# Kernel optimization log

Hardware: AMD Instinct MI355X
Metric: run time of the kernel (lower is better)

## Reference

```python
import jax, jax.numpy as jnp
import numpy as np

N = 40000
E = 640000
D_RNA = 1000
D_PROT = 300
H = 64      # hidden_channels
OUT = 32    # out_channels
HEADS = 4


def setup_inputs() -> dict:
    key = jax.random.key(0)
    ks = jax.random.split(key, 24)
    s = 0.05
    w = lambda k, shape: jax.random.normal(k, shape, jnp.float32) * s
    inp = {
        'x': jax.random.normal(ks[0], (N, D_RNA + D_PROT), jnp.float32),
        'edge_index': jax.random.randint(ks[1], (2, E), 0, N, jnp.int32),
        'input_dim_rna': D_RNA,
        # embeddings
        'W_rna': w(ks[2], (D_RNA, H)), 'b_rna': jnp.zeros((H,), jnp.float32),
        'W_prot': w(ks[3], (D_PROT, H)), 'b_prot': jnp.zeros((H,), jnp.float32),
        # GATConv1: in 2H=128 -> heads*H=256
        'W1s': w(ks[4], (2 * H, HEADS * H)), 'W1d': w(ks[5], (2 * H, HEADS * H)),
        'att1_s': w(ks[6], (HEADS, H)), 'att1_d': w(ks[7], (HEADS, H)),
        'bias1': jnp.zeros((HEADS * H,), jnp.float32),
        # lin1: 2H -> heads*H
        'Wl1': w(ks[8], (2 * H, HEADS * H)), 'bl1': jnp.zeros((HEADS * H,), jnp.float32),
        # GATConv2: in heads*H=256 -> heads*OUT=128
        'W2s': w(ks[9], (HEADS * H, HEADS * OUT)), 'W2d': w(ks[10], (HEADS * H, HEADS * OUT)),
        'att2_s': w(ks[11], (HEADS, OUT)), 'att2_d': w(ks[12], (HEADS, OUT)),
        'bias2': jnp.zeros((HEADS * OUT,), jnp.float32),
        # lin2: heads*H -> heads*OUT
        'Wl2': w(ks[13], (HEADS * H, HEADS * OUT)), 'bl2': jnp.zeros((HEADS * OUT,), jnp.float32),
    }
    return inp


def _gat(x_in, edge_index, Ws, Wd, att_s, att_d, bias, heads, ch):
    # PyG GATConv, bipartite weights, add_self_loops=False, concat=True, eval (no dropout)
    n = x_in.shape[0]
    src, dst = edge_index[0], edge_index[1]
    xs = (x_in @ Ws).reshape(n, heads, ch)   # source projection
    xd = (x_in @ Wd).reshape(n, heads, ch)   # destination projection
    a_s = jnp.einsum('nhc,hc->nh', xs, att_s)  # [N,H]
    a_d = jnp.einsum('nhc,hc->nh', xd, att_d)  # [N,H]
    e = jax.nn.leaky_relu(a_s[src] + a_d[dst], 0.2)          # [E,H]
    m = jax.lax.stop_gradient(jax.ops.segment_max(e, dst, num_segments=n))
    p = jnp.exp(e - m[dst])
    denom = jax.ops.segment_sum(p, dst, num_segments=n)       # [N,H]
    alpha = p / denom[dst]                                    # segment softmax over incoming edges
    msg = xs[src] * alpha[:, :, None]                         # [E,H,C]
    agg = jax.ops.segment_sum(msg, dst, num_segments=n)       # [N,H,C]
    return agg.reshape(n, heads * ch) + bias


def reference(x, edge_index, input_dim_rna, W_rna, b_rna, W_prot, b_prot,
              W1s, W1d, att1_s, att1_d, bias1, Wl1, bl1,
              W2s, W2d, att2_s, att2_d, bias2, Wl2, bl2):
    x_rna = x[:, :input_dim_rna] @ W_rna + b_rna
    x_prot = x[:, input_dim_rna:] @ W_prot + b_prot
    h = jnp.concatenate([x_rna, x_prot], axis=1)              # [N, 2H]
    h = _gat(h, edge_index, W1s, W1d, att1_s, att1_d, bias1, HEADS, H) + h @ Wl1 + bl1
    h = jax.nn.relu(h)
    out = _gat(h, edge_index, W2s, W2d, att2_s, att2_d, bias2, HEADS, OUT) + h @ Wl2 + bl2
    return out
```

## Files before the change

kernel.cpp:

```cpp
#include <hip/hip_runtime.h>
#include <hip/hip_bf16.h>
#include <stdint.h>


#define HEADS 4
#define CH1   64
#define CH2   32
#define HC1   256
#define HC2   128

static constexpr int D_RNA  = 1000;
static constexpr int D_PROT = 300;
static constexpr int D_IN   = 1300;
static constexpr int HDIM   = 128;

typedef __bf16 bf16x8 __attribute__((ext_vector_type(8)));
typedef float  f32x4  __attribute__((ext_vector_type(4)));
typedef unsigned short ushort;

__device__ __forceinline__ float lrelu(float x) { return x >= 0.f ? x : 0.2f * x; }
__device__ __forceinline__ float bf2f(unsigned int u16) {
  return __uint_as_float(u16 << 16);
}
__device__ __forceinline__ ushort f2bf(float f) {
  union { float f; unsigned int u; } x; x.f = f;
  unsigned int r = x.u + 0x7fffu + ((x.u >> 16) & 1u);
  return (ushort)(r >> 16);
}

__global__ void zero_i32(int* p, int n) {
  int i = blockIdx.x * 256 + threadIdx.x;
  if (i < n) p[i] = 0;
}

__global__ void hist_kernel(const int* __restrict__ dstv, int* __restrict__ deg, int E) {
  int i = blockIdx.x * 256 + threadIdx.x;
  if (i < E) atomicAdd(&deg[dstv[i]], 1);
}

__global__ void scan_kernel(const int* __restrict__ deg, int* __restrict__ off,
                            int* __restrict__ cur, int n) {
  __shared__ int s[1024];
  int tid = threadIdx.x;
  const int CHK = (n + 1023) / 1024;
  int base = tid * CHK;
  int sum = 0;
  for (int j = 0; j < CHK; ++j) {
    int i = base + j;
    if (i < n) sum += deg[i];
  }
  s[tid] = sum;
  __syncthreads();
  for (int o = 1; o < 1024; o <<= 1) {
    int t = (tid >= o) ? s[tid - o] : 0;
    __syncthreads();
    s[tid] += t;
    __syncthreads();
  }
  int run = s[tid] - sum;
  for (int j = 0; j < CHK; ++j) {
    int i = base + j;
    if (i < n) {
      off[i] = run; cur[i] = run;
      run += deg[i];
    }
  }
  if (tid == 1023) off[n] = s[1023];
}

__global__ void scatter_kernel(const int* __restrict__ srcv, const int* __restrict__ dstv,
                               int* __restrict__ cur, int* __restrict__ srcs, int E) {
  int i = blockIdx.x * 256 + threadIdx.x;
  if (i < E) {
    int d = dstv[i];
    int pos = atomicAdd(&cur[d], 1);
    srcs[pos] = srcv[i];
  }
}

__global__ void fold_att_kernel(const float* __restrict__ W1s, const float* __restrict__ W1d,
                                const float* __restrict__ at1s, const float* __restrict__ at1d,
                                const float* __restrict__ W2s, const float* __restrict__ W2d,
                                const float* __restrict__ at2s, const float* __restrict__ at2d,
                                ushort* __restrict__ BTA1, ushort* __restrict__ BTA2) {
  int tid = blockIdx.x * blockDim.x + threadIdx.x;
  int stride = gridDim.x * blockDim.x;
  for (int o = tid; o < HDIM * HEADS; o += stride) {
    int k = o >> 2, h = o & 3;
    float ss = 0.f, sd = 0.f;
    for (int c = 0; c < CH1; ++c) {
      ss += W1s[k * HC1 + h * CH1 + c] * at1s[h * CH1 + c];
      sd += W1d[k * HC1 + h * CH1 + c] * at1d[h * CH1 + c];
    }
    ushort sh = f2bf(ss), dh = f2bf(sd);
    BTA1[(0 + h) * HDIM + k] = sh;
    BTA1[(4 + h) * HDIM + k] = f2bf(ss - bf2f(sh));
    BTA1[(8 + h) * HDIM + k] = dh;
    BTA1[(12 + h) * HDIM + k] = f2bf(sd - bf2f(dh));
  }
  for (int o = tid; o < HC1 * HEADS; o += stride) {
    int k = o >> 2, h = o & 3;
    float ss = 0.f, sd = 0.f;
    for (int c = 0; c < CH2; ++c) {
      ss += W2s[k * HC2 + h * CH2 + c] * at2s[h * CH2 + c];
      sd += W2d[k * HC2 + h * CH2 + c] * at2d[h * CH2 + c];
    }
    ushort sh = f2bf(ss), dh = f2bf(sd);
    BTA2[(0 + h) * HC1 + k] = sh;
    BTA2[(4 + h) * HC1 + k] = f2bf(ss - bf2f(sh));
    BTA2[(8 + h) * HC1 + k] = dh;
    BTA2[(12 + h) * HC1 + k] = f2bf(sd - bf2f(dh));
  }
  for (int i = tid; i < 48 * HDIM; i += stride) BTA1[16 * HDIM + i] = 0;
  for (int i = tid; i < 48 * HC1; i += stride) BTA2[16 * HC1 + i] = 0;
}

__global__ void convert_weights(const float* __restrict__ W_rna, const float* __restrict__ W_prot,
                                const float* __restrict__ W1s, const float* __restrict__ Wl1,
                                const float* __restrict__ W2s, const float* __restrict__ Wl2,
                                const float* __restrict__ b1, const float* __restrict__ bl1,
                                const float* __restrict__ b2, const float* __restrict__ bl2,
                                ushort* BTr, ushort* BTp, ushort* BT1, ushort* BT2,
                                float* biasL1, float* biasL2) {
  int tid = blockIdx.x * blockDim.x + threadIdx.x;
  int stride = gridDim.x * blockDim.x;
  for (int i = tid; i < 64 * 1024; i += stride) {
    int n = i >> 10, k = i & 1023;
    BTr[i] = (k < D_RNA) ? f2bf(W_rna[k * 64 + n]) : 0;
  }
  for (int i = tid; i < 64 * 320; i += stride) {
    int n = i / 320, k = i - n * 320;
    BTp[i] = (k < D_PROT) ? f2bf(W_prot[k * 64 + n]) : 0;
  }
  for (int i = tid; i < 512 * 128; i += stride) {
    int n = i >> 7, k = i & 127;
    BT1[i] = f2bf(n < 256 ? W1s[k * 256 + n] : Wl1[k * 256 + n - 256]);
  }
  for (int i = tid; i < 256 * 256; i += stride) {
    int n = i >> 8, k = i & 255;
    BT2[i] = f2bf(n < 128 ? W2s[k * 128 + n] : Wl2[k * 128 + n - 128]);
  }
  for (int i = tid; i < 512; i += stride) biasL1[i] = (i < 256) ? b1[i] : bl1[i - 256];
  for (int i = tid; i < 256; i += stride) biasL2[i] = (i < 128) ? b2[i] : bl2[i - 128];
}

#define LDK 72

__device__ __forceinline__ f32x4 mfma_bf16(bf16x8 a, bf16x8 b, f32x4 c) {
  return __builtin_amdgcn_mfma_f32_16x16x32_bf16(a, b, c, 0, 0, 0);
}

__launch_bounds__(256)
__global__ void embed_gemm(const float* __restrict__ x,
                           const ushort* __restrict__ BTr, const ushort* __restrict__ BTp,
                           const float* __restrict__ b_rna, const float* __restrict__ b_prot,
                           ushort* __restrict__ h0) {
  const bool prot = (blockIdx.x == 1);
  const int Kpad = prot ? 320 : 1024;
  const int acol = prot ? D_RNA : 0;
  const ushort* BT = prot ? BTp : BTr;
  const float* bias = prot ? b_prot : b_rna;
  const int r0 = blockIdx.y * 64;

  __shared__ ushort As[64 * LDK];
  __shared__ ushort Bs[64 * LDK];
  int tid = threadIdx.x;
  int wave = tid >> 6, lane = tid & 63;
  int quad = lane >> 4, lr = lane & 15;
  f32x4 acc[4];
#pragma unroll
  for (int c = 0; c < 4; ++c) acc[c] = (f32x4){0.f, 0.f, 0.f, 0.f};

  int srow = tid >> 2, skq = (tid & 3) * 16;
  const float* aprow = x + (size_t)(r0 + srow) * D_IN;
  const ushort* bprow = BT + (size_t)srow * Kpad;

  float4 fa[4];
  uint4 fb0, fb1;

  auto loadA = [&](int k0) {
#pragma unroll
    for (int q = 0; q < 4; ++q) {
      int kg = acol + k0 + skq + q * 4;
      fa[q] = (kg + 4 <= D_IN) ? *(const float4*)(aprow + kg)
                               : make_float4(0.f, 0.f, 0.f, 0.f);
    }
  };
  auto loadB = [&](int k0) {
    const ushort* bp = bprow + k0 + skq;
    fb0 = *(const uint4*)bp;
    fb1 = *(const uint4*)(bp + 8);
  };

  loadA(0);
  loadB(0);

  for (int k0 = 0; k0 < Kpad; k0 += 64) {
    {
      ushort tmp[16];
#pragma unroll
      for (int q = 0; q < 4; ++q) {
        tmp[q * 4 + 0] = f2bf(fa[q].x); tmp[q * 4 + 1] = f2bf(fa[q].y);
        tmp[q * 4 + 2] = f2bf(fa[q].z); tmp[q * 4 + 3] = f2bf(fa[q].w);
      }
      *(uint4*)&As[srow * LDK + skq] = *(const uint4*)&tmp[0];
      *(uint4*)&As[srow * LDK + skq + 8] = *(const uint4*)&tmp[8];
      *(uint4*)&Bs[srow * LDK + skq] = fb0;
      *(uint4*)&Bs[srow * LDK + skq + 8] = fb1;
    }
    __syncthreads();
    if (k0 + 64 < Kpad) {
      loadA(k0 + 64);
      loadB(k0 + 64);
    }
    int arow = wave * 16 + lr;
    bf16x8 a0 = *(const bf16x8*)&As[arow * LDK + quad * 8];
    bf16x8 a1 = *(const bf16x8*)&As[arow * LDK + 32 + quad * 8];
#pragma unroll
    for (int c = 0; c < 4; ++c) {
      bf16x8 b0 = *(const bf16x8*)&Bs[(c * 16 + lr) * LDK + quad * 8];
      bf16x8 b1 = *(const bf16x8*)&Bs[(c * 16 + lr) * LDK + 32 + quad * 8];
      acc[c] = mfma_bf16(a0, b0, acc[c]);
      acc[c] = mfma_bf16(a1, b1, acc[c]);
    }
    __syncthreads();
  }
  int colb = prot ? 64 : 0;
#pragma unroll
  for (int c = 0; c < 4; ++c) {
#pragma unroll
    for (int j = 0; j < 4; ++j) {
      int row = r0 + wave * 16 + quad * 4 + j;
      int col = c * 16 + lr;
      h0[(size_t)row * HDIM + colb + col] = f2bf(acc[c][j] + bias[col]);
    }
  }
}

__launch_bounds__(256)
__global__ void layer_gemm(const ushort* __restrict__ A, int K,
                           const ushort* __restrict__ BT, const float* __restrict__ bias,
                           ushort* __restrict__ out0, ushort* __restrict__ out1, int halfw,
                           const ushort* __restrict__ BTA,
                           float* __restrict__ a_s, float* __restrict__ a_d) {
  const bool att = (blockIdx.x == gridDim.x - 1);
  const int cb = att ? 0 : blockIdx.x * 128;
  const int r0 = blockIdx.y * 64;
  __shared__ ushort As[64 * LDK];
  __shared__ ushort Bs[2][64 * LDK];
  int tid = threadIdx.x;
  int wave = tid >> 6, lane = tid & 63;
  int quad = lane >> 4, lr = lane & 15;
  f32x4 acc[8];
#pragma unroll
  for (int c = 0; c < 8; ++c) acc[c] = (f32x4){0.f, 0.f, 0.f, 0.f};

  int srow = tid >> 2, skq = (tid & 3) * 16;
  const ushort* aprow = A + (size_t)(r0 + srow) * K;
  const ushort* bprow0 = att ? (BTA + (size_t)srow * K)
                             : (BT + (size_t)(cb + srow) * K);
  const ushort* bprow1 = BT + (size_t)(cb + 64 + srow) * K;

  uint4 fa0, fa1, fb00, fb01, fb10, fb11;
  auto loadAB = [&](int k0) {
    const ushort* ap = aprow + k0 + skq;
    fa0 = *(const uint4*)ap;
    fa1 = *(const uint4*)(ap + 8);
    const ushort* bp0 = bprow0 + k0 + skq;
    fb00 = *(const uint4*)bp0;
    fb01 = *(const uint4*)(bp0 + 8);
    if (!att) {
      const ushort* bp1 = bprow1 + k0 + skq;
      fb10 = *(const uint4*)bp1;
      fb11 = *(const uint4*)(bp1 + 8);
    }
  };

  loadAB(0);

  for (int k0 = 0; k0 < K; k0 += 64) {
    *(uint4*)&As[srow * LDK + skq] = fa0;
    *(uint4*)&As[srow * LDK + skq + 8] = fa1;
    *(uint4*)&Bs[0][srow * LDK + skq] = fb00;
    *(uint4*)&Bs[0][srow * LDK + skq + 8] = fb01;
    if (!att) {
      *(uint4*)&Bs[1][srow * LDK + skq] = fb10;
      *(uint4*)&Bs[1][srow * LDK + skq + 8] = fb11;
    }
    __syncthreads();
    if (k0 + 64 < K) loadAB(k0 + 64);
    int arow = wave * 16 + lr;
    bf16x8 a0 = *(const bf16x8*)&As[arow * LDK + quad * 8];
    bf16x8 a1 = *(const bf16x8*)&As[arow * LDK + 32 + quad * 8];
#pragma unroll
    for (int c = 0; c < 4; ++c) {
      bf16x8 b0 = *(const bf16x8*)&Bs[0][(c * 16 + lr) * LDK + quad * 8];
      bf16x8 b1 = *(const bf16x8*)&Bs[0][(c * 16 + lr) * LDK + 32 + quad * 8];
      acc[c] = mfma_bf16(a0, b0, acc[c]);
      acc[c] = mfma_bf16(a1, b1, acc[c]);
    }
    if (!att) {
#pragma unroll
      for (int c = 0; c < 4; ++c) {
        bf16x8 b0 = *(const bf16x8*)&Bs[1][(c * 16 + lr) * LDK + quad * 8];
        bf16x8 b1 = *(const bf16x8*)&Bs[1][(c * 16 + lr) * LDK + 32 + quad * 8];
        acc[4 + c] = mfma_bf16(a0, b0, acc[4 + c]);
        acc[4 + c] = mfma_bf16(a1, b1, acc[4 + c]);
      }
    }
    __syncthreads();
  }
  if (att) {
#pragma unroll
    for (int j = 0; j < 4; ++j) {
      int row = r0 + wave * 16 + quad * 4 + j;
      float v0 = acc[0][j];
      float sum = v0 + __shfl_xor(v0, 4);
      if (lr < 4)                    a_s[(size_t)row * 4 + lr] = sum;
      else if (lr >= 8 && lr < 12)   a_d[(size_t)row * 4 + (lr - 8)] = sum;
    }
    return;
  }
#pragma unroll
  for (int t = 0; t < 2; ++t) {
#pragma unroll
    for (int c = 0; c < 4; ++c) {
#pragma unroll
      for (int j = 0; j < 4; ++j) {
        int row = r0 + wave * 16 + quad * 4 + j;
        int cg = cb + t * 64 + c * 16 + lr;
        ushort v = f2bf(acc[t * 4 + c][j] + bias[cg]);
        if (cg < halfw) out0[(size_t)row * halfw + cg] = v;
        else            out1[(size_t)row * halfw + cg - halfw] = v;
      }
    }
  }
}

__device__ __forceinline__ void load_bf8(const ushort* p, float* o) {
  uint4 q = *(const uint4*)p;
  o[0] = bf2f(q.x & 0xffffu); o[1] = bf2f(q.x >> 16);
  o[2] = bf2f(q.y & 0xffffu); o[3] = bf2f(q.y >> 16);
  o[4] = bf2f(q.z & 0xffffu); o[5] = bf2f(q.z >> 16);
  o[6] = bf2f(q.w & 0xffffu); o[7] = bf2f(q.w >> 16);
}

template <int CH, bool RELU, bool OUT_BF16>
__launch_bounds__(256)
__global__ void gat_fused_kernel(const int* __restrict__ off, const int* __restrict__ srcs,
                                 const float* __restrict__ a_s, const float* __restrict__ a_d,
                                 const ushort* __restrict__ xs,
                                 const float* __restrict__ bias,
                                 const ushort* __restrict__ skip,
                                 void* __restrict__ outv, int N) {
  const int HC  = 4 * CH;
  const int LPH = CH / 8;
  const int LPN = 4 * LPH;
  const int NPW = 64 / LPN;
  int wave = threadIdx.x >> 6, lane = threadIdx.x & 63;
  int g  = lane / LPN;
  int hl = (lane % LPN) / LPH;
  int li = lane % LPH;
  int n = blockIdx.x * (4 * NPW) + wave * NPW + g;
  if (n >= N) return;
  int i = off[n], end = off[n + 1];
  float adn = a_d[(size_t)n * 4 + hl];
  const int cofs = hl * CH + li * 8;

  float m = -1e30f, s = 0.f;
  float acc[8];
#pragma unroll
  for (int v = 0; v < 8; ++v) acc[v] = 0.f;

  for (; i + 2 <= end; i += 2) {
    int sA = srcs[i], sB = srcs[i + 1];
    float eA = lrelu(a_s[(size_t)sA * 4 + hl] + adn);
    float eB = lrelu(a_s[(size_t)sB * 4 + hl] + adn);
    float xA[8], xB[8];
    load_bf8(xs + (size_t)sA * HC + cofs, xA);
    load_bf8(xs + (size_t)sB * HC + cofs, xB);
    float mn = fmaxf(m, fmaxf(eA, eB));
    if (mn > m) {
      float f = __expf(m - mn);
      s *= f;
#pragma unroll
      for (int v = 0; v < 8; ++v) acc[v] *= f;
      m = mn;
    }
    float pA = __expf(eA - m), pB = __expf(eB - m);
    s += pA + pB;
#pragma unroll
    for (int v = 0; v < 8; ++v) acc[v] += pA * xA[v] + pB * xB[v];
  }
  if (i < end) {
    int sA = srcs[i];
    float eA = lrelu(a_s[(size_t)sA * 4 + hl] + adn);
    float xA[8];
    load_bf8(xs + (size_t)sA * HC + cofs, xA);
    if (eA > m) {
      float f = __expf(m - eA);
      s *= f;
#pragma unroll
      for (int v = 0; v < 8; ++v) acc[v] *= f;
      m = eA;
    }
    float pA = __expf(eA - m);
    s += pA;
#pragma unroll
    for (int v = 0; v < 8; ++v) acc[v] += pA * xA[v];
  }

  float r = s > 0.f ? 1.f / s : 0.f;
  size_t obase = (size_t)n * HC + cofs;
  float sk[8];
  load_bf8(skip + obase, sk);
  float val[8];
#pragma unroll
  for (int v = 0; v < 8; ++v) {
    val[v] = acc[v] * r + bias[cofs + v] + sk[v];
    if (RELU) val[v] = fmaxf(val[v], 0.f);
  }
  if (OUT_BF16) {
    ushort o8[8];
#pragma unroll
    for (int v = 0; v < 8; ++v) o8[v] = f2bf(val[v]);
    *(uint4*)&((ushort*)outv)[obase] = *(const uint4*)o8;
  } else {
    float* op = (float*)outv + obase;
    *(float4*)op = make_float4(val[0], val[1], val[2], val[3]);
    *(float4*)(op + 4) = make_float4(val[4], val[5], val[6], val[7]);
  }
}

extern "C" void kernel_launch(void* const* d_in, const int* in_sizes, int n_in,
                              void* d_out, int out_size, void* d_ws, size_t ws_size,
                              hipStream_t stream) {
  const float* x      = (const float*)d_in[0];
  const int*   ei     = (const int*)d_in[1];
  const float* W_rna  = (const float*)d_in[3];
  const float* b_rna  = (const float*)d_in[4];
  const float* W_prot = (const float*)d_in[5];
  const float* b_prot = (const float*)d_in[6];
  const float* W1s    = (const float*)d_in[7];
  const float* W1d    = (const float*)d_in[8];
  const float* at1s   = (const float*)d_in[9];
  const float* at1d   = (const float*)d_in[10];
  const float* bias1  = (const float*)d_in[11];
  const float* Wl1    = (const float*)d_in[12];
  const float* bl1    = (const float*)d_in[13];
  const float* W2s    = (const float*)d_in[14];
  const float* W2d    = (const float*)d_in[15];
  const float* at2s   = (const float*)d_in[16];
  const float* at2d   = (const float*)d_in[17];
  const float* bias2  = (const float*)d_in[18];
  const float* Wl2    = (const float*)d_in[19];
  const float* bl2    = (const float*)d_in[20];

  const int N = in_sizes[0] / D_IN;
  const int E = in_sizes[1] / 2;
  const int* srcv = ei;
  const int* dstv = ei + E;

  char* ws = (char*)d_ws;
  size_t o = 0;
  auto carve = [&](size_t bytes) {
    void* p = ws + o;
    o += (bytes + 255) & ~(size_t)255;
    return p;
  };
  int* deg    = (int*)carve((size_t)N * 4);
  int* offp   = (int*)carve((size_t)(N + 1) * 4);
  int* cur    = (int*)carve((size_t)N * 4);
  int* srcs   = (int*)carve((size_t)E * 4);
  float* a_s  = (float*)carve((size_t)N * 4 * 4);
  float* a_d  = (float*)carve((size_t)N * 4 * 4);
  ushort* BTr = (ushort*)carve(64 * 1024 * 2);
  ushort* BTp = (ushort*)carve(64 * 320 * 2);
  ushort* BT1 = (ushort*)carve(512 * 128 * 2);
  ushort* BT2 = (ushort*)carve(256 * 256 * 2);
  ushort* BTA1 = (ushort*)carve(64 * 128 * 2);
  ushort* BTA2 = (ushort*)carve(64 * 256 * 2);
  float* biasL1 = (float*)carve(512 * 4);
  float* biasL2 = (float*)carve(256 * 4);
  ushort* h0  = (ushort*)carve((size_t)N * HDIM * 2);
  ushort* xs1 = (ushort*)carve((size_t)N * HC1 * 2);
  ushort* z1  = (ushort*)carve((size_t)N * HC1 * 2);
  ushort* h1  = (ushort*)carve((size_t)N * HC1 * 2);
  ushort* xs2 = h0;
  ushort* z2  = z1;
  float* out = (float*)d_out;

  zero_i32<<<(N + 255) / 256, 256, 0, stream>>>(deg, N);
  hist_kernel<<<(E + 255) / 256, 256, 0, stream>>>(dstv, deg, E);
  scan_kernel<<<1, 1024, 0, stream>>>(deg, offp, cur, N);
  scatter_kernel<<<(E + 255) / 256, 256, 0, stream>>>(srcv, dstv, cur, srcs, E);
  fold_att_kernel<<<8, 256, 0, stream>>>(W1s, W1d, at1s, at1d, W2s, W2d, at2s, at2d,
                                         BTA1, BTA2);
  convert_weights<<<256, 256, 0, stream>>>(W_rna, W_prot, W1s, Wl1, W2s, Wl2,
                                           bias1, bl1, bias2, bl2,
                                           BTr, BTp, BT1, BT2, biasL1, biasL2);
  embed_gemm<<<dim3(2, N / 64), 256, 0, stream>>>(x, BTr, BTp, b_rna, b_prot, h0);
  layer_gemm<<<dim3(5, N / 64), 256, 0, stream>>>(h0, HDIM, BT1, biasL1, xs1, z1, HC1,
                                                  BTA1, a_s, a_d);
  gat_fused_kernel<CH1, true, true><<<N / 8, 256, 0, stream>>>(offp, srcs, a_s, a_d, xs1,
                                                               bias1, z1, h1, N);
  layer_gemm<<<dim3(3, N / 64), 256, 0, stream>>>(h1, HC1, BT2, biasL2, xs2, z2, HC2,
                                                  BTA2, a_s, a_d);
  gat_fused_kernel<CH2, false, false><<<N / 16, 256, 0, stream>>>(offp, srcs, a_s, a_d, xs2,
                                                                  bias2, z2, out, N);
}
```

Measured before the change: 655.5 us.

## Split embed GEMM K dimension across two thread groups with shared-memory reduction

The embedding GEMM block grows from 256 to 512 threads, and two 256-thread groups each handle half of the K range with their own LDS tiles. The partial sums are then combined through shared memory before bias and store. The protein weight padding grows from 320 to 384 so K splits evenly into 64-wide chunks. The aim is to double the parallelism and memory-level concurrency on this bandwidth-heavy stage, at the cost of more LDS, a reduction pass, and a little wasted padded K work.

New measurement: 679.0 us. 3.6% more time.

```diff
diff --git a/kernel.cpp b/kernel.cpp
--- a/kernel.cpp
+++ b/kernel.cpp
@@ -128,8 +128,8 @@
     int n = i >> 10, k = i & 1023;
     BTr[i] = (k < D_RNA) ? f2bf(W_rna[k * 64 + n]) : 0;
   }
-  for (int i = tid; i < 64 * 320; i += stride) {
-    int n = i / 320, k = i - n * 320;
+  for (int i = tid; i < 64 * 384; i += stride) {
+    int n = i / 384, k = i - n * 384;
     BTp[i] = (k < D_PROT) ? f2bf(W_prot[k * 64 + n]) : 0;
   }
   for (int i = tid; i < 512 * 128; i += stride) {
@@ -150,30 +150,36 @@
   return __builtin_amdgcn_mfma_f32_16x16x32_bf16(a, b, c, 0, 0, 0);
 }
 
-__launch_bounds__(256)
+__launch_bounds__(512)
 __global__ void embed_gemm(const float* __restrict__ x,
                            const ushort* __restrict__ BTr, const ushort* __restrict__ BTp,
                            const float* __restrict__ b_rna, const float* __restrict__ b_prot,
                            ushort* __restrict__ h0) {
   const bool prot = (blockIdx.x == 1);
-  const int Kpad = prot ? 320 : 1024;
-  const int acol = prot ? D_RNA : 0;
+  const int Kpad  = prot ? 384 : 1024;
+  const int Khalf = Kpad >> 1;
+  const int iters = Khalf >> 6;
+  const int acol  = prot ? D_RNA : 0;
   const ushort* BT = prot ? BTp : BTr;
   const float* bias = prot ? b_prot : b_rna;
   const int r0 = blockIdx.y * 64;
 
-  __shared__ ushort As[64 * LDK];
-  __shared__ ushort Bs[64 * LDK];
+  __shared__ ushort As[2][64 * LDK];
+  __shared__ ushort Bs[2][64 * LDK];
   int tid = threadIdx.x;
-  int wave = tid >> 6, lane = tid & 63;
+  int g = tid >> 8;
+  int t = tid & 255;
+  int wave = t >> 6, lane = tid & 63;
   int quad = lane >> 4, lr = lane & 15;
+  const int kbase = g * Khalf;
+
   f32x4 acc[4];
 #pragma unroll
   for (int c = 0; c < 4; ++c) acc[c] = (f32x4){0.f, 0.f, 0.f, 0.f};
 
-  int srow = tid >> 2, skq = (tid & 3) * 16;
+  int srow = t >> 2, skq = (t & 3) * 16;
   const float* aprow = x + (size_t)(r0 + srow) * D_IN;
-  const ushort* bprow = BT + (size_t)srow * Kpad;
+  const ushort* bprow = BT + (size_t)srow * Kpad + kbase;
 
   float4 fa[4];
   uint4 fb0, fb1;
@@ -181,9 +187,9 @@
   auto loadA = [&](int k0) {
 #pragma unroll
     for (int q = 0; q < 4; ++q) {
-      int kg = acol + k0 + skq + q * 4;
-      fa[q] = (kg + 4 <= D_IN) ? *(const float4*)(aprow + kg)
-                               : make_float4(0.f, 0.f, 0.f, 0.f);
+      int col = acol + kbase + k0 + skq + q * 4;
+      fa[q] = (col + 4 <= D_IN) ? *(const float4*)(aprow + col)
+                                : make_float4(0.f, 0.f, 0.f, 0.f);
     }
   };
   auto loadB = [&](int k0) {
@@ -195,7 +201,7 @@
   loadA(0);
   loadB(0);
 
-  for (int k0 = 0; k0 < Kpad; k0 += 64) {
+  for (int it = 0; it < iters; ++it) {
     {
       ushort tmp[16];
 #pragma unroll
@@ -203,36 +209,52 @@
         tmp[q * 4 + 0] = f2bf(fa[q].x); tmp[q * 4 + 1] = f2bf(fa[q].y);
         tmp[q * 4 + 2] = f2bf(fa[q].z); tmp[q * 4 + 3] = f2bf(fa[q].w);
       }
-      *(uint4*)&As[srow * LDK + skq] = *(const uint4*)&tmp[0];
-      *(uint4*)&As[srow * LDK + skq + 8] = *(const uint4*)&tmp[8];
-      *(uint4*)&Bs[srow * LDK + skq] = fb0;
-      *(uint4*)&Bs[srow * LDK + skq + 8] = fb1;
+      *(uint4*)&As[g][srow * LDK + skq] = *(const uint4*)&tmp[0];
+      *(uint4*)&As[g][srow * LDK + skq + 8] = *(const uint4*)&tmp[8];
+      *(uint4*)&Bs[g][srow * LDK + skq] = fb0;
+      *(uint4*)&Bs[g][srow * LDK + skq + 8] = fb1;
     }
     __syncthreads();
-    if (k0 + 64 < Kpad) {
-      loadA(k0 + 64);
-      loadB(k0 + 64);
+    if (it + 1 < iters) {
+      loadA((it + 1) * 64);
+      loadB((it + 1) * 64);
     }
     int arow = wave * 16 + lr;
-    bf16x8 a0 = *(const bf16x8*)&As[arow * LDK + quad * 8];
-    bf16x8 a1 = *(const bf16x8*)&As[arow * LDK + 32 + quad * 8];
+    bf16x8 a0 = *(const bf16x8*)&As[g][arow * LDK + quad * 8];
+    bf16x8 a1 = *(const bf16x8*)&As[g][arow * LDK + 32 + quad * 8];
 #pragma unroll
     for (int c = 0; c < 4; ++c) {
-      bf16x8 b0 = *(const bf16x8*)&Bs[(c * 16 + lr) * LDK + quad * 8];
-      bf16x8 b1 = *(const bf16x8*)&Bs[(c * 16 + lr) * LDK + 32 + quad * 8];
+      bf16x8 b0 = *(const bf16x8*)&Bs[g][(c * 16 + lr) * LDK + quad * 8];
+      bf16x8 b1 = *(const bf16x8*)&Bs[g][(c * 16 + lr) * LDK + 32 + quad * 8];
       acc[c] = mfma_bf16(a0, b0, acc[c]);
       acc[c] = mfma_bf16(a1, b1, acc[c]);
     }
     __syncthreads();
   }
-  int colb = prot ? 64 : 0;
-#pragma unroll
-  for (int c = 0; c < 4; ++c) {
-#pragma unroll
-    for (int j = 0; j < 4; ++j) {
-      int row = r0 + wave * 16 + quad * 4 + j;
-      int col = c * 16 + lr;
-      h0[(size_t)row * HDIM + colb + col] = f2bf(acc[c][j] + bias[col]);
+
+  float* red = (float*)&As[0][0];
+  if (g == 1) {
+#pragma unroll
+    for (int c = 0; c < 4; ++c) {
+#pragma unroll
+      for (int j = 0; j < 4; ++j) {
+        int row_l = wave * 16 + quad * 4 + j;
+        red[row_l * 65 + c * 16 + lr] = acc[c][j];
+      }
+    }
+  }
+  __syncthreads();
+  if (g == 0) {
+    int colb = prot ? 64 : 0;
+#pragma unroll
+    for (int c = 0; c < 4; ++c) {
+#pragma unroll
+      for (int j = 0; j < 4; ++j) {
+        int row_l = wave * 16 + quad * 4 + j;
+        int col = c * 16 + lr;
+        float v = acc[c][j] + red[row_l * 65 + col] + bias[col];
+        h0[(size_t)(r0 + row_l) * HDIM + colb + col] = f2bf(v);
+      }
     }
   }
 }
@@ -475,7 +497,7 @@
   float* a_s  = (float*)carve((size_t)N * 4 * 4);
   float* a_d  = (float*)carve((size_t)N * 4 * 4);
   ushort* BTr = (ushort*)carve(64 * 1024 * 2);
-  ushort* BTp = (ushort*)carve(64 * 320 * 2);
+  ushort* BTp = (ushort*)carve(64 * 384 * 2);
   ushort* BT1 = (ushort*)carve(512 * 128 * 2);
   ushort* BT2 = (ushort*)carve(256 * 256 * 2);
   ushort* BTA1 = (ushort*)carve(64 * 128 * 2);
@@ -499,7 +521,7 @@
   convert_weights<<<256, 256, 0, stream>>>(W_rna, W_prot, W1s, Wl1, W2s, Wl2,
                                            bias1, bl1, bias2, bl2,
                                            BTr, BTp, BT1, BT2, biasL1, biasL2);
-  embed_gemm<<<dim3(2, N / 64), 256, 0, stream>>>(x, BTr, BTp, b_rna, b_prot, h0);
+  embed_gemm<<<dim3(2, N / 64), 512, 0, stream>>>(x, BTr, BTp, b_rna, b_prot, h0);
   layer_gemm<<<dim3(5, N / 64), 256, 0, stream>>>(h0, HDIM, BT1, biasL1, xs1, z1, HC1,
                                                   BTA1, a_s, a_d);
   gat_fused_kernel<CH1, true, true><<<N / 8, 256, 0, stream>>>(offp, srcs, a_s, a_d, xs1,
```

## Split each node's edge list across two lane groups in GAT aggregation

Applied to the files above, without the earlier changes.

Each destination node's incoming edges are now split between two lane groups, one taking the even edges and one the odd edges, each running its own online softmax. The partial max, sum and accumulators are merged with cross-lane shuffles, and only the first group writes the output. The grid doubles so each wave handles half as many nodes. This aims to shorten the serial edge loop per node and raise memory-level parallelism for the gathers. The cost is the shuffle merge and idle lanes in the epilogue.

After: 653.3 us. No clear change (-0.3%).

```diff
diff --git a/kernel.cpp b/kernel.cpp
--- a/kernel.cpp
+++ b/kernel.cpp
@@ -355,15 +355,19 @@
                                  void* __restrict__ outv, int N) {
   const int HC  = 4 * CH;
   const int LPH = CH / 8;
-  const int LPN = 4 * LPH;
+  const int CLN = 4 * LPH;
+  const int LPN = 2 * CLN;
   const int NPW = 64 / LPN;
   int wave = threadIdx.x >> 6, lane = threadIdx.x & 63;
-  int g  = lane / LPN;
-  int hl = (lane % LPN) / LPH;
-  int li = lane % LPH;
+  int g   = lane / LPN;
+  int rem = lane % LPN;
+  int es  = rem / CLN;
+  int cl  = rem % CLN;
+  int hl  = cl / LPH;
+  int li  = cl % LPH;
   int n = blockIdx.x * (4 * NPW) + wave * NPW + g;
   if (n >= N) return;
-  int i = off[n], end = off[n + 1];
+  int s0 = off[n], end = off[n + 1];
   float adn = a_d[(size_t)n * 4 + hl];
   const int cofs = hl * CH + li * 8;
 
@@ -372,27 +376,29 @@
 #pragma unroll
   for (int v = 0; v < 8; ++v) acc[v] = 0.f;
 
-  for (; i + 2 <= end; i += 2) {
-    int sA = srcs[i], sB = srcs[i + 1];
-    float eA = lrelu(a_s[(size_t)sA * 4 + hl] + adn);
-    float eB = lrelu(a_s[(size_t)sB * 4 + hl] + adn);
+  int i = s0 + es;
+  for (; i + 2 < end; i += 4) {
+    int sA = srcs[i], sB = srcs[i + 2];
+    float eA = a_s[(size_t)sA * 4 + hl];
+    float eB = a_s[(size_t)sB * 4 + hl];
     float xA[8], xB[8];
     load_bf8(xs + (size_t)sA * HC + cofs, xA);
     load_bf8(xs + (size_t)sB * HC + cofs, xB);
-    float mn = fmaxf(m, fmaxf(eA, eB));
-    if (mn > m) {
-      float f = __expf(m - mn);
+    eA = lrelu(eA + adn); eB = lrelu(eB + adn);
+    float em = fmaxf(eA, eB);
+    if (em > m) {
+      float f = __expf(m - em);
       s *= f;
 #pragma unroll
       for (int v = 0; v < 8; ++v) acc[v] *= f;
-      m = mn;
+      m = em;
     }
     float pA = __expf(eA - m), pB = __expf(eB - m);
     s += pA + pB;
 #pragma unroll
     for (int v = 0; v < 8; ++v) acc[v] += pA * xA[v] + pB * xB[v];
   }
-  if (i < end) {
+  for (; i < end; i += 2) {
     int sA = srcs[i];
     float eA = lrelu(a_s[(size_t)sA * 4 + hl] + adn);
     float xA[8];
@@ -409,6 +415,19 @@
 #pragma unroll
     for (int v = 0; v < 8; ++v) acc[v] += pA * xA[v];
   }
+
+  {
+    float m2 = fmaxf(m, __shfl_xor(m, CLN));
+    float f = __expf(m - m2);
+    s *= f;
+    s += __shfl_xor(s, CLN);
+#pragma unroll
+    for (int v = 0; v < 8; ++v) {
+      acc[v] *= f;
+      acc[v] += __shfl_xor(acc[v], CLN);
+    }
+  }
+  if (es != 0) return;
 
   float r = s > 0.f ? 1.f / s : 0.f;
   size_t obase = (size_t)n * HC + cofs;
@@ -502,10 +521,10 @@
   embed_gemm<<<dim3(2, N / 64), 256, 0, stream>>>(x, BTr, BTp, b_rna, b_prot, h0);
   layer_gemm<<<dim3(5, N / 64), 256, 0, stream>>>(h0, HDIM, BT1, biasL1, xs1, z1, HC1,
                                                   BTA1, a_s, a_d);
-  gat_fused_kernel<CH1, true, true><<<N / 8, 256, 0, stream>>>(offp, srcs, a_s, a_d, xs1,
+  gat_fused_kernel<CH1, true, true><<<N / 4, 256, 0, stream>>>(offp, srcs, a_s, a_d, xs1,
                                                                bias1, z1, h1, N);
   layer_gemm<<<dim3(3, N / 64), 256, 0, stream>>>(h1, HC1, BT2, biasL2, xs2, z2, HC2,
                                                   BTA2, a_s, a_d);
-  gat_fused_kernel<CH2, false, false><<<N / 16, 256, 0, stream>>>(offp, srcs, a_s, a_d, xs2,
-                                                                  bias2, z2, out, N);
-}
+  gat_fused_kernel<CH2, false, false><<<N / 8, 256, 0, stream>>>(offp, srcs, a_s, a_d, xs2,
+                                                                 bias2, z2, out, N);
+}
```
